# Kernel optimization log

Measured on AMD Instinct MI355X. Metric: run time of the kernel, lower is better.

Reference implementation:

```python
import jax, jax.numpy as jnp
import numpy as np


def setup_inputs() -> dict:
    key = jax.random.key(0)
    ks = jax.random.split(key, 12)
    Tq, Tk, B, H = 1024, 1024, 8, 1024
    inp = {
        "inputs_q": jax.random.normal(ks[0], (Tq, B, H), jnp.float32),
        "inputs_kv": jax.random.normal(ks[1], (Tk, B, H), jnp.float32),
        "w_q": jax.random.normal(ks[2], (H, H), jnp.float32) * 0.02,
        "b_q": jnp.zeros((H,), jnp.float32),
        "w_kv": jax.random.normal(ks[3], (2 * H, H), jnp.float32) * 0.02,
        "b_kv": jnp.zeros((2 * H,), jnp.float32),
        "w_o": jax.random.normal(ks[4], (H, H), jnp.float32) * 0.02,
        "b_o": jnp.zeros((H,), jnp.float32),
        # BatchEnsemble rank-1 factors, initialized near 1
        "r_q": 1.0 + 0.05 * jax.random.normal(ks[5], (B, H), jnp.float32),
        "s_q": 1.0 + 0.05 * jax.random.normal(ks[6], (B, H), jnp.float32),
        "r_kv": 1.0 + 0.05 * jax.random.normal(ks[7], (B, H), jnp.float32),
        "s_kv": 1.0 + 0.05 * jax.random.normal(ks[8], (B, 2 * H), jnp.float32),
        "heads": 16,
    }
    return inp


def be_linear(x, w, b, r, s):
    # x: [T,B,Hin], w: [Hout,Hin], r: [B,Hin], s: [B,Hout]
    return jnp.einsum('tbh,oh->tbo', x * r, w) * s + b


def reference(inputs_q, inputs_kv, w_q, b_q, w_kv, b_kv, w_o, b_o,
              r_q, s_q, r_kv, s_kv, heads):
    Tq, B, H = inputs_q.shape
    Tk = inputs_kv.shape[0]
    hd = H // heads
    scale = hd ** -0.5

    q = be_linear(inputs_q, w_q, b_q, r_q, s_q)          # [Tq,B,H]
    kv = be_linear(inputs_kv, w_kv, b_kv, r_kv, s_kv)    # [Tk,B,2H]

    queries = q.reshape(Tq, B * heads, hd)
    kv = kv.reshape(Tk, B * heads, 2, hd)                # layout: head x {k,v} x hd
    keys = kv[:, :, 0, :]
    values = kv[:, :, 1, :]

    scores = jnp.einsum('qnd,knd->nqk', queries, keys) * scale  # [B*heads,Tq,Tk]
    probs = jax.nn.softmax(scores.astype(jnp.float32), axis=-1).astype(scores.dtype)
    # dropout_prob = 0 / eval: dropout is identity
    ctx = jnp.einsum('nqk,knd->qnd', probs, values).reshape(Tq, B, H)
    out = jnp.einsum('tbh,oh->tbo', ctx, w_o) + b_o      # [Tq,B,H]
    return out
```

## Files before the change

kernel.cpp:

```cpp
#include <hip/hip_runtime.h>
#include <stdint.h>

typedef unsigned short u16;
typedef __bf16 bf16x8 __attribute__((ext_vector_type(8)));
typedef float f32x4 __attribute__((ext_vector_type(4)));

typedef __attribute__((address_space(3))) void lds_void;
typedef const __attribute__((address_space(1))) void gbl_void;
#define GLD_LDS16(g, l) __builtin_amdgcn_global_load_lds((gbl_void*)(g), (lds_void*)(l), 16, 0, 0)

__device__ __forceinline__ u16 f2bf(float f) {
  unsigned u = __float_as_uint(f);
  u += 0x7fffu + ((u >> 16) & 1u);
  return (u16)(u >> 16);
}

__device__ __forceinline__ unsigned pk2bf(float a, float b) {
  unsigned au = __float_as_uint(a) + 0x8000u;
  unsigned bu = __float_as_uint(b) + 0x8000u;
  return __builtin_amdgcn_perm(bu, au, 0x07060302u);
}

__global__ void k_convert_all(const float* __restrict__ inq, const float* __restrict__ r_q,
                              const float* __restrict__ inkv, const float* __restrict__ r_kv,
                              const float* __restrict__ w_q, const float* __restrict__ w_kv,
                              const float* __restrict__ w_o,
                              u16* __restrict__ Xq, u16* __restrict__ Xkv,
                              u16* __restrict__ Wq, u16* __restrict__ Wkv,
                              u16* __restrict__ Wo) {
  int blk = blockIdx.x;
  const float* src; const float* r = nullptr; u16* dst; int base;
  if (blk < 8192)       { src = inq;  r = r_q;  dst = Xq;  base = 0; }
  else if (blk < 16384) { src = inkv; r = r_kv; dst = Xkv; base = 8192; }
  else if (blk < 17408) { src = w_q;  dst = Wq;  base = 16384; }
  else if (blk < 19456) { src = w_kv; dst = Wkv; base = 17408; }
  else                  { src = w_o;  dst = Wo;  base = 19456; }
  int i4 = ((blk - base) * 256 + threadIdx.x) * 4;
  float4 xv = *(const float4*)(src + i4);
  if (r) {
    int rb = ((i4 >> 10) & 7) * 1024 + (i4 & 1023);
    float4 rv = *(const float4*)(r + rb);
    xv.x *= rv.x; xv.y *= rv.y; xv.z *= rv.z; xv.w *= rv.w;
  }
  unsigned long long pk = (unsigned long long)pk2bf(xv.x, xv.y)
      | ((unsigned long long)pk2bf(xv.z, xv.w) << 32);
  *(unsigned long long*)(dst + i4) = pk;
}

template <int MODE>
__global__ void k_gemm_bt(const u16* __restrict__ A, const u16* __restrict__ B,
                          void* __restrict__ Cout, const float* __restrict__ s,
                          const float* __restrict__ bias, int M, int N, int K,
                          float postscale) {
  __shared__ __align__(16) u16 As[128 * 32];
  __shared__ __align__(16) u16 Bs[128 * 32];
  const int tid = threadIdx.x;
  const int w = tid >> 6, lane = tid & 63;
  const int quad = lane >> 4, l16 = lane & 15;
  const int n0 = blockIdx.x * 128, m0 = blockIdx.y * 128;
  const int wm = (w & 1) * 64, wn = (w >> 1) * 64;

  f32x4 acc[4][4] = {};

  int srow[2], scol[2];
#pragma unroll
  for (int i = 0; i < 2; ++i) {
    int p = (w * 2 + i) * 64 + lane;
    int row = p >> 2;
    int cb = (p & 3) ^ ((row >> 1) & 3);
    srow[i] = row; scol[i] = cb * 8;
  }
  int offA[4], offB[4];
#pragma unroll
  for (int t = 0; t < 4; ++t) {
    int ra = wm + t * 16 + l16;
    offA[t] = ra * 32 + ((quad ^ ((ra >> 1) & 3)) * 8);
    int rb = wn + t * 16 + l16;
    offB[t] = rb * 32 + ((quad ^ ((rb >> 1) & 3)) * 8);
  }

  for (int k0 = 0; k0 < K; k0 += 32) {
#pragma unroll
    for (int i = 0; i < 2; ++i) {
      GLD_LDS16(A + (size_t)(m0 + srow[i]) * K + k0 + scol[i], As + (w * 2 + i) * 512);
      GLD_LDS16(B + (size_t)(n0 + srow[i]) * K + k0 + scol[i], Bs + (w * 2 + i) * 512);
    }
    __syncthreads();
    bf16x8 af[4], bfr[4];
#pragma unroll
    for (int mt = 0; mt < 4; ++mt) af[mt] = *(const bf16x8*)(As + offA[mt]);
#pragma unroll
    for (int nt = 0; nt < 4; ++nt) bfr[nt] = *(const bf16x8*)(Bs + offB[nt]);
#pragma unroll
    for (int mt = 0; mt < 4; ++mt)
#pragma unroll
      for (int nt = 0; nt < 4; ++nt)
        acc[mt][nt] = __builtin_amdgcn_mfma_f32_16x16x32_bf16(af[mt], bfr[nt], acc[mt][nt], 0, 0, 0);
    __syncthreads();
  }

#pragma unroll
  for (int mt = 0; mt < 4; ++mt)
#pragma unroll
    for (int nt = 0; nt < 4; ++nt) {
      int n = n0 + wn + nt * 16 + l16;
#pragma unroll
      for (int rg = 0; rg < 4; ++rg) {
        int m = m0 + wm + mt * 16 + quad * 4 + rg;
        float v = acc[mt][nt][rg];
        if (MODE == 0) {
          v = (v * s[(m & 7) * N + n] + bias[n]) * postscale;
          ((u16*)Cout)[(size_t)m * N + n] = f2bf(v);
        } else {
          ((float*)Cout)[(size_t)m * N + n] = v + bias[n];
        }
      }
    }
}

__global__ void k_transpose_v(const u16* __restrict__ kv, u16* __restrict__ vt) {
  __shared__ __align__(16) u16 tile[64][72];
  const int tid = threadIdx.x;
  const int n = blockIdx.x >> 4;
  const int t0 = (blockIdx.x & 15) << 6;
#pragma unroll
  for (int it = 0; it < 2; ++it) {
    int r = it * 32 + (tid >> 3);
    int c = (tid & 7) << 3;
    *(uint4*)&tile[r][c] = *(const uint4*)(kv + ((size_t)(t0 + r) * 128 + n) * 128 + 64 + c);
  }
  __syncthreads();
#pragma unroll
  for (int it = 0; it < 2; ++it) {
    int d = it * 32 + (tid >> 3);
    int tc = (tid & 7) << 3;
    u16 v[8];
#pragma unroll
    for (int j = 0; j < 8; ++j) v[j] = tile[tc + j][d];
    uint4 o;
    o.x = (unsigned)v[0] | ((unsigned)v[1] << 16);
    o.y = (unsigned)v[2] | ((unsigned)v[3] << 16);
    o.z = (unsigned)v[4] | ((unsigned)v[5] << 16);
    o.w = (unsigned)v[6] | ((unsigned)v[7] << 16);
    *(uint4*)(vt + ((size_t)n * 64 + d) * 1024 + t0 + tc) = o;
  }
}

__global__ __launch_bounds__(512, 4) void k_attn(const u16* __restrict__ qb,
                                                 const u16* __restrict__ kvb,
                                                 const u16* __restrict__ vtb,
                                                 u16* __restrict__ ctx) {
  __shared__ __align__(16) u16 Ks[64 * 64];
  __shared__ __align__(16) u16 Vts[64 * 64];
  __shared__ __align__(16) u16 Ps[8][16 * 72];

  const int tid = threadIdx.x;
  const int w = tid >> 6, lane = tid & 63;
  const int quad = lane >> 4, l16 = lane & 15;
  const int n = blockIdx.x >> 3;
  const int q0 = (blockIdx.x & 7) << 7;
  const int tq = q0 + w * 16 + l16;

  bf16x8 bq[2];
#pragma unroll
  for (int ks = 0; ks < 2; ++ks)
    bq[ks] = *(const bf16x8*)(qb + ((size_t)tq * 128 + n) * 64 + ks * 32 + quad * 8);

  const int wv = w & 3;
  int sr[2], scb[2];
#pragma unroll
  for (int i = 0; i < 2; ++i) {
    int p = (wv * 2 + i) * 64 + lane;
    sr[i] = p >> 3;
    scb[i] = ((p & 7) ^ (sr[i] & 7)) * 8;
  }

  float l_i = 0.f;
  f32x4 accO[4] = {};
  u16* myP = Ps[w];
  const int pbase = l16 * 72;

#pragma unroll 1
  for (int tk0 = 0; tk0 < 1024; tk0 += 64) {
#pragma unroll
    for (int i = 0; i < 2; ++i) {
      if (w < 4) {
        GLD_LDS16(kvb + ((size_t)(tk0 + sr[i]) * 128 + n) * 128 + scb[i],
                  Ks + (wv * 2 + i) * 512);
      } else {
        GLD_LDS16(vtb + ((size_t)n * 64 + sr[i]) * 1024 + tk0 + scb[i],
                  Vts + (wv * 2 + i) * 512);
      }
    }
    __syncthreads();

    f32x4 accS[4] = {};
#pragma unroll
    for (int mt = 0; mt < 4; ++mt) {
      int r = mt * 16 + l16;
#pragma unroll
      for (int ks = 0; ks < 2; ++ks) {
        bf16x8 ak = *(const bf16x8*)(Ks + r * 64 + (((ks * 4 + quad) ^ (r & 7)) << 3));
        accS[mt] = __builtin_amdgcn_mfma_f32_16x16x32_bf16(ak, bq[ks], accS[mt], 0, 0, 0);
      }
    }

    float pv[16];
    float ssum = 0.f;
#pragma unroll
    for (int mt = 0; mt < 4; ++mt)
#pragma unroll
      for (int rg = 0; rg < 4; ++rg) {
        float p = __builtin_amdgcn_exp2f(accS[mt][rg]);
        pv[mt * 4 + rg] = p;
        ssum += p;
      }
    ssum += __shfl_xor(ssum, 16);
    ssum += __shfl_xor(ssum, 32);
    l_i += ssum;

#pragma unroll
    for (int mt = 0; mt < 4; ++mt) {
      unsigned long long pk = (unsigned long long)pk2bf(pv[mt * 4 + 0], pv[mt * 4 + 1])
          | ((unsigned long long)pk2bf(pv[mt * 4 + 2], pv[mt * 4 + 3]) << 32);
      *(unsigned long long*)(myP + pbase + mt * 16 + quad * 4) = pk;
    }
#pragma unroll
    for (int dt = 0; dt < 4; ++dt) {
      int r = dt * 16 + l16;
#pragma unroll
      for (int ks = 0; ks < 2; ++ks) {
        bf16x8 av = *(const bf16x8*)(Vts + r * 64 + (((ks * 4 + quad) ^ (r & 7)) << 3));
        bf16x8 bp = *(const bf16x8*)(myP + pbase + ks * 32 + quad * 8);
        accO[dt] = __builtin_amdgcn_mfma_f32_16x16x32_bf16(av, bp, accO[dt], 0, 0, 0);
      }
    }
    __syncthreads();
  }

  float inv = 1.f / l_i;
#pragma unroll
  for (int dt = 0; dt < 4; ++dt) {
    unsigned long long pk = (unsigned long long)pk2bf(accO[dt][0] * inv, accO[dt][1] * inv)
        | ((unsigned long long)pk2bf(accO[dt][2] * inv, accO[dt][3] * inv) << 32);
    *(unsigned long long*)(ctx + ((size_t)tq * 128 + n) * 64 + dt * 16 + quad * 4) = pk;
  }
}

extern "C" void kernel_launch(void* const* d_in, const int* in_sizes, int n_in,
                              void* d_out, int out_size, void* d_ws, size_t ws_size,
                              hipStream_t stream) {
  const float* inq  = (const float*)d_in[0];
  const float* inkv = (const float*)d_in[1];
  const float* w_q  = (const float*)d_in[2];
  const float* b_q  = (const float*)d_in[3];
  const float* w_kv = (const float*)d_in[4];
  const float* b_kv = (const float*)d_in[5];
  const float* w_o  = (const float*)d_in[6];
  const float* b_o  = (const float*)d_in[7];
  const float* r_q  = (const float*)d_in[8];
  const float* s_q  = (const float*)d_in[9];
  const float* r_kv = (const float*)d_in[10];
  const float* s_kv = (const float*)d_in[11];

  const size_t MEG = 1024 * 1024;
  u16* ws    = (u16*)d_ws;
  u16* Xq    = ws;
  u16* Xkv   = ws + 8 * MEG;
  u16* Wq    = ws + 16 * MEG;
  u16* Wkv   = ws + 17 * MEG;
  u16* Wo    = ws + 19 * MEG;
  u16* qbuf  = ws + 20 * MEG;
  u16* kvbuf = ws + 28 * MEG;
  u16* vt    = Xkv;
  u16* ctx   = Xq;

  k_convert_all<<<20480, 256, 0, stream>>>(inq, r_q, inkv, r_kv, w_q, w_kv, w_o,
                                           Xq, Xkv, Wq, Wkv, Wo);

  const float QSCALE = 0.125f * 1.44269504088896340736f;
  k_gemm_bt<0><<<dim3(8, 64), 256, 0, stream>>>(Xq, Wq, qbuf, s_q, b_q, 8192, 1024, 1024, QSCALE);
  k_gemm_bt<0><<<dim3(16, 64), 256, 0, stream>>>(Xkv, Wkv, kvbuf, s_kv, b_kv, 8192, 2048, 1024, 1.0f);
  k_transpose_v<<<2048, 256, 0, stream>>>(kvbuf, vt);
  k_attn<<<1024, 512, 0, stream>>>(qbuf, kvbuf, vt, ctx);
  k_gemm_bt<1><<<dim3(8, 64), 256, 0, stream>>>(ctx, Wo, d_out, nullptr, b_o, 8192, 1024, 1024, 1.0f);
}
```

Before: 306.2 us.

## Double-buffer K/V tiles in attention and remap blocks for head locality

The attention kernel now keeps two LDS buffers for the K and V^T tiles. The next tile's load is issued right after a single barrier, so it overlaps with the current tile's MFMA work, and the trailing barrier is dropped. The block index is remapped so the head index varies fastest, which places all query tiles of one head on the same XCD under round-robin dispatch and should improve L2 reuse. The softmax row sum is split into two accumulators to shorten the dependency chain. The doubled K/V buffers raise LDS use per block, which may lower the number of resident blocks per CU.

```diff
diff --git a/kernel.cpp b/kernel.cpp
--- a/kernel.cpp
+++ b/kernel.cpp
@@ -150,15 +150,15 @@
                                                  const u16* __restrict__ kvb,
                                                  const u16* __restrict__ vtb,
                                                  u16* __restrict__ ctx) {
-  __shared__ __align__(16) u16 Ks[64 * 64];
-  __shared__ __align__(16) u16 Vts[64 * 64];
+  __shared__ __align__(16) u16 Ks[2][64 * 64];
+  __shared__ __align__(16) u16 Vts[2][64 * 64];
   __shared__ __align__(16) u16 Ps[8][16 * 72];
 
   const int tid = threadIdx.x;
   const int w = tid >> 6, lane = tid & 63;
   const int quad = lane >> 4, l16 = lane & 15;
-  const int n = blockIdx.x >> 3;
-  const int q0 = (blockIdx.x & 7) << 7;
+  const int n = blockIdx.x & 127;
+  const int q0 = (blockIdx.x >> 7) << 7;
   const int tq = q0 + w * 16 + l16;
 
   bf16x8 bq[2];
@@ -175,24 +175,44 @@
     scb[i] = ((p & 7) ^ (sr[i] & 7)) * 8;
   }
 
+  const bool isK = (w < 4);
+  const u16* gbase[2];
+  u16* lbase[2];
+#pragma unroll
+  for (int i = 0; i < 2; ++i) {
+    if (isK) {
+      gbase[i] = kvb + ((size_t)sr[i] * 128 + n) * 128 + scb[i];
+      lbase[i] = &Ks[0][(wv * 2 + i) * 512];
+    } else {
+      gbase[i] = vtb + ((size_t)n * 64 + sr[i]) * 1024 + scb[i];
+      lbase[i] = &Vts[0][(wv * 2 + i) * 512];
+    }
+  }
+  const size_t gstep = isK ? 16384 : 1;
+  const int lstep = 64 * 64;
+
   float l_i = 0.f;
   f32x4 accO[4] = {};
   u16* myP = Ps[w];
   const int pbase = l16 * 72;
 
+#pragma unroll
+  for (int i = 0; i < 2; ++i) GLD_LDS16(gbase[i], lbase[i]);
+
 #pragma unroll 1
   for (int tk0 = 0; tk0 < 1024; tk0 += 64) {
-#pragma unroll
-    for (int i = 0; i < 2; ++i) {
-      if (w < 4) {
-        GLD_LDS16(kvb + ((size_t)(tk0 + sr[i]) * 128 + n) * 128 + scb[i],
-                  Ks + (wv * 2 + i) * 512);
-      } else {
-        GLD_LDS16(vtb + ((size_t)n * 64 + sr[i]) * 1024 + tk0 + scb[i],
-                  Vts + (wv * 2 + i) * 512);
-      }
-    }
+    const int cur = (tk0 >> 6) & 1;
     __syncthreads();
+
+    if (tk0 < 960) {
+      size_t goff = (size_t)(tk0 + 64) * gstep;
+#pragma unroll
+      for (int i = 0; i < 2; ++i)
+        GLD_LDS16(gbase[i] + goff, lbase[i] + (cur ^ 1) * lstep);
+    }
+
+    const u16* Kc = Ks[cur];
+    const u16* Vc = Vts[cur];
 
     f32x4 accS[4] = {};
 #pragma unroll
@@ -200,21 +220,22 @@
       int r = mt * 16 + l16;
 #pragma unroll
       for (int ks = 0; ks < 2; ++ks) {
-        bf16x8 ak = *(const bf16x8*)(Ks + r * 64 + (((ks * 4 + quad) ^ (r & 7)) << 3));
+        bf16x8 ak = *(const bf16x8*)(Kc + r * 64 + (((ks * 4 + quad) ^ (r & 7)) << 3));
         accS[mt] = __builtin_amdgcn_mfma_f32_16x16x32_bf16(ak, bq[ks], accS[mt], 0, 0, 0);
       }
     }
 
     float pv[16];
-    float ssum = 0.f;
+    float s0 = 0.f, s1 = 0.f;
 #pragma unroll
     for (int mt = 0; mt < 4; ++mt)
 #pragma unroll
       for (int rg = 0; rg < 4; ++rg) {
         float p = __builtin_amdgcn_exp2f(accS[mt][rg]);
         pv[mt * 4 + rg] = p;
-        ssum += p;
+        if (rg & 1) s1 += p; else s0 += p;
       }
+    float ssum = s0 + s1;
     ssum += __shfl_xor(ssum, 16);
     ssum += __shfl_xor(ssum, 32);
     l_i += ssum;
@@ -230,12 +251,11 @@
       int r = dt * 16 + l16;
 #pragma unroll
       for (int ks = 0; ks < 2; ++ks) {
-        bf16x8 av = *(const bf16x8*)(Vts + r * 64 + (((ks * 4 + quad) ^ (r & 7)) << 3));
+        bf16x8 av = *(const bf16x8*)(Vc + r * 64 + (((ks * 4 + quad) ^ (r & 7)) << 3));
         bf16x8 bp = *(const bf16x8*)(myP + pbase + ks * 32 + quad * 8);
         accO[dt] = __builtin_amdgcn_mfma_f32_16x16x32_bf16(av, bp, accO[dt], 0, 0, 0);
       }
     }
-    __syncthreads();
   }
 
   float inv = 1.f / l_i;
```

Result: slower. 314.8 us (+2.8%).
